# Performance work log

Hardware: AMD Instinct MI355X
Metric: run time of the kernel (lower is better)

The kernel has to match this reference:

```python
import jax, jax.numpy as jnp
import numpy as np

B, LAT, FCON, NCOND = 1024, 64, 256, 1
HID, E, GATE_H = 512, 8, 64
FREC, NFUT = 256, 2
IN_SZ = LAT + FCON * NCOND          # 320
INTER = LAT + HID                   # 576
OUT_SZ = NFUT * FREC                # 512


def setup_inputs() -> dict:
    key = jax.random.key(0)
    ks = jax.random.split(key, 16)

    def kaiming(k, shape):
        # kaiming_uniform over fan_in = shape[-2] (matches torch init on [E, in, out])
        fan_in = shape[-2]
        bound = np.sqrt(6.0 / fan_in)
        return jax.random.uniform(k, shape, jnp.float32, -bound, bound)

    def lin(kw, kb, din, dout):
        bound = 1.0 / np.sqrt(din)
        w = jax.random.uniform(kw, (din, dout), jnp.float32, -bound, bound)
        b = jax.random.uniform(kb, (dout,), jnp.float32, -bound, bound)
        return w, b

    gw1, gb1 = lin(ks[0], ks[1], IN_SZ, GATE_H)
    gw2, gb2 = lin(ks[2], ks[3], GATE_H, GATE_H)
    gw3, gb3 = lin(ks[4], ks[5], GATE_H, E)

    return {
        "z": jax.random.normal(ks[6], (B, LAT), jnp.float32),
        "c": jax.random.normal(ks[7], (B, FCON * NCOND), jnp.float32),
        "w0": kaiming(ks[8], (E, IN_SZ, HID)),
        "b0": jnp.full((E, HID), 0.01, jnp.float32),
        "w1": kaiming(ks[9], (E, INTER, HID)),
        "b1": jnp.full((E, HID), 0.01, jnp.float32),
        "w2": kaiming(ks[10], (E, INTER, OUT_SZ)),
        "b2": jnp.full((E, OUT_SZ), 0.01, jnp.float32),
        "gw1": gw1, "gb1": gb1,
        "gw2": gw2, "gb2": gb2,
        "gw3": gw3, "gb3": gb3,
    }


def _moe_layer(coeff, z, layer_out, w, b, act):
    # math identical to: mixed_w = coeff @ flat(w); baddbmm(mixed_b, inp, mixed_w)
    # expressed as a fused contraction (no [B, in, out] materialization)
    inp = jnp.concatenate((z, layer_out), axis=1)          # [B, in]
    out = jnp.einsum('bi,eio,be->bo', inp, w, coeff)       # [B, out]
    out = out + coeff @ b                                  # mixed bias
    return act(out) if act is not None else out


def reference(z, c, w0, b0, w1, b1, w2, b2, gw1, gb1, gw2, gb2, gw3, gb3):
    x = jnp.concatenate((z, c), axis=1)                    # [B, IN_SZ]
    h = jax.nn.elu(x @ gw1 + gb1)
    h = jax.nn.elu(h @ gw2 + gb2)
    coeff = jax.nn.softmax(h @ gw3 + gb3, axis=1)          # [B, E]

    out = _moe_layer(coeff, z, c, w0, b0, jax.nn.elu)      # [B, HID]
    out = _moe_layer(coeff, z, out, w1, b1, jax.nn.elu)    # [B, HID]
    out = _moe_layer(coeff, z, out, w2, b2, None)          # [B, OUT_SZ]
    return out
```

## Files before the change

### kernel.cpp

```cpp
#include <hip/hip_runtime.h>
#include <hip/hip_bf16.h>
#include <stdint.h>
#include <math.h>

#define B_    1024
#define LAT   64
#define FCON  256
#define IN_SZ 320
#define HID   512
#define E_    8
#define GH    64
#define INTER 576
#define OUT_SZ 512
#define NTOT  4096
#define KI0   10
#define KI12  18

typedef __attribute__((ext_vector_type(8))) __bf16 bf16x8;
typedef __attribute__((ext_vector_type(4))) float  f32x4;

__device__ __forceinline__ float elu_f(float x) { return x > 0.f ? x : expf(x) - 1.f; }
__device__ __forceinline__ __bf16 to_bf16(float f) {
    __hip_bfloat16 h = __float2bfloat16(f);
    return *reinterpret_cast<__bf16*>(&h);
}


#define PREP_ZC   160
#define PREP_W0   (PREP_ZC + KI0 * 64)
#define PREP_W1   (PREP_W0 + KI12 * 64)
#define PREP_W2   (PREP_W1 + KI12 * 64)
#define PREP_ALL  (PREP_W2 + 256)

__device__ __forceinline__ void do_zcpack(
    int bx, const float* __restrict__ z, const float* __restrict__ c,
    bf16x8* __restrict__ Ap0, bf16x8* __restrict__ Ap1, bf16x8* __restrict__ Ap2)
{
    const int wid  = bx * 4 + (threadIdx.x >> 6);
    const int lane = threadIdx.x & 63, q = lane >> 4, r = lane & 15;
    bf16x8 v;
    if (wid < 128) {
        const int mi = wid >> 1, ki = wid & 1;
        const float* src = z + (size_t)(mi * 16 + r) * LAT + ki * 32 + q * 8;
        const f32x4 lo = *(const f32x4*)src, hi = *(const f32x4*)(src + 4);
#pragma unroll
        for (int j = 0; j < 4; j++) { v[j] = to_bf16(lo[j]); v[j + 4] = to_bf16(hi[j]); }
        Ap0[((size_t)mi * KI0  + ki) * 64 + lane] = v;
        Ap1[((size_t)mi * KI12 + ki) * 64 + lane] = v;
        Ap2[((size_t)mi * KI12 + ki) * 64 + lane] = v;
    } else {
        const int cid = wid - 128;
        const int mi = cid >> 3, ki = 2 + (cid & 7);
        const float* src = c + (size_t)(mi * 16 + r) * FCON + (ki - 2) * 32 + q * 8;
        const f32x4 lo = *(const f32x4*)src, hi = *(const f32x4*)(src + 4);
#pragma unroll
        for (int j = 0; j < 4; j++) { v[j] = to_bf16(lo[j]); v[j + 4] = to_bf16(hi[j]); }
        Ap0[((size_t)mi * KI0 + ki) * 64 + lane] = v;
    }
}

__device__ __forceinline__ void do_wpack(
    int f, const float* __restrict__ w, bf16x8* __restrict__ Wp, int KI)
{
    const int ki = f % KI;
    const int ni = (f / KI) * 4 + (threadIdx.x >> 6);
    const int lane = threadIdx.x & 63, q = lane >> 4, r = lane & 15;
    const int n = ni * 16 + r, e = n >> 9, o = n & 511;
    const int K = KI * 32;
    const float* src = w + (size_t)e * K * 512 + (size_t)(ki * 32 + q * 8) * 512 + o;
    bf16x8 v;
#pragma unroll
    for (int j = 0; j < 8; j++) v[j] = to_bf16(src[(size_t)j * 512]);
    Wp[((size_t)ni * KI + ki) * 64 + lane] = v;
}

__global__ __launch_bounds__(256) void prep_kernel(
    const float* __restrict__ z, const float* __restrict__ c,
    const float* __restrict__ w0, const float* __restrict__ w1,
    const float* __restrict__ w2,
    const float* __restrict__ gw1, const float* __restrict__ gb1,
    const float* __restrict__ gw2, const float* __restrict__ gb2,
    const float* __restrict__ gw3, const float* __restrict__ gb3,
    bf16x8* __restrict__ Ap0, bf16x8* __restrict__ Ap1, bf16x8* __restrict__ Ap2,
    bf16x8* __restrict__ Wp0, bf16x8* __restrict__ Wp1, bf16x8* __restrict__ Wp2,
    float* __restrict__ coeff)
{
    const int bx = blockIdx.x;
    if (bx < PREP_ZC) {
        do_zcpack(bx, z, c, Ap0, Ap1, Ap2);
    } else if (bx < PREP_W0) {
        do_wpack(bx - PREP_ZC, w0, Wp0, KI0);
    } else if (bx < PREP_W1) {
        do_wpack(bx - PREP_W0, w1, Wp1, KI12);
    } else if (bx < PREP_W2) {
        do_wpack(bx - PREP_W1, w2, Wp2, KI12);
    } else {
        __shared__ float h[4][GH];
        __shared__ float lg[4][E_];
        const int lane = threadIdx.x & 63, wave = threadIdx.x >> 6;
        const int row = (bx - PREP_W2) * 4 + wave;
        const float* zr = z + (size_t)row * LAT;
        const float* cr = c + (size_t)row * FCON;

        float a1 = gb1[lane];
        for (int i = 0; i < LAT; i++)  a1 = fmaf(zr[i], gw1[i * GH + lane], a1);
        for (int i = 0; i < FCON; i++) a1 = fmaf(cr[i], gw1[(LAT + i) * GH + lane], a1);
        h[wave][lane] = elu_f(a1);
        __syncthreads();

        float a2 = gb2[lane];
        for (int i = 0; i < GH; i++) a2 = fmaf(h[wave][i], gw2[i * GH + lane], a2);
        a2 = elu_f(a2);
        __syncthreads();
        h[wave][lane] = a2;
        __syncthreads();

        if (lane < E_) {
            float a3 = gb3[lane];
            for (int i = 0; i < GH; i++) a3 = fmaf(h[wave][i], gw3[i * E_ + lane], a3);
            lg[wave][lane] = a3;
        }
        __syncthreads();
        if (lane < E_) {
            float mx = lg[wave][0];
            for (int i = 1; i < E_; i++) mx = fmaxf(mx, lg[wave][i]);
            float s = 0.f;
            for (int i = 0; i < E_; i++) s += expf(lg[wave][i] - mx);
            coeff[(size_t)row * E_ + lane] = expf(lg[wave][lane] - mx) / s;
        }
    }
}

template<int KI, int FINAL>
__global__ __launch_bounds__(256) void layer_kernel(
    const bf16x8* __restrict__ Ap, const bf16x8* __restrict__ Wp,
    const float* __restrict__ coeff, const float* __restrict__ bias,
    __bf16* __restrict__ ApN, float* __restrict__ fout)
{
    const int lane = threadIdx.x & 63, w = threadIdx.x >> 6;
    const int q = lane >> 4, r = lane & 15;
    const int o0 = blockIdx.x * 16;
    const int nt = blockIdx.x;
    const int mi0 = blockIdx.y * 8 + w * 2;

    const bf16x8* aB0 = Ap + (size_t)(mi0 + 0) * KI * 64 + lane;
    const bf16x8* aB1 = Ap + (size_t)(mi0 + 1) * KI * 64 + lane;
    const bf16x8* bBase = Wp + (size_t)nt * KI * 64 + lane;

    f32x4 acc[2][E_];
#pragma unroll
    for (int u = 0; u < 2; u++)
#pragma unroll
        for (int e = 0; e < E_; e++) acc[u][e] = (f32x4){0.f, 0.f, 0.f, 0.f};

#pragma unroll
    for (int ki = 0; ki < KI; ++ki) {
        const bf16x8 af0 = aB0[(size_t)ki * 64];
        const bf16x8 af1 = aB1[(size_t)ki * 64];
        bf16x8 bf[E_];
#pragma unroll
        for (int e = 0; e < E_; e++)
            bf[e] = bBase[((size_t)e * 32 * KI + ki) * 64];
#pragma unroll
        for (int e = 0; e < E_; e++) {
            acc[0][e] = __builtin_amdgcn_mfma_f32_16x16x32_bf16(af0, bf[e], acc[0][e], 0, 0, 0);
            acc[1][e] = __builtin_amdgcn_mfma_f32_16x16x32_bf16(af1, bf[e], acc[1][e], 0, 0, 0);
        }
    }

    float be[E_];
#pragma unroll
    for (int e = 0; e < E_; e++) be[e] = bias[(size_t)e * 512 + o0 + r];

#pragma unroll
    for (int u = 0; u < 2; u++) {
        const int mi = mi0 + u;
#pragma unroll
        for (int v = 0; v < 4; v++) {
            const int row = mi * 16 + q * 4 + v;
            const float* cr = coeff + (size_t)row * E_;
            const f32x4 clo = *(const f32x4*)cr, chi = *(const f32x4*)(cr + 4);
            float s = 0.f;
#pragma unroll
            for (int e = 0; e < 4; e++) s += clo[e] * (acc[u][e][v] + be[e]);
#pragma unroll
            for (int e = 0; e < 4; e++) s += chi[e] * (acc[u][4 + e][v] + be[4 + e]);
            if (FINAL) {
                fout[(size_t)row * OUT_SZ + o0 + r] = s;
            } else {
                const float h = elu_f(s);
                const int k  = LAT + o0 + r;
                const int ki2 = k >> 5, kq2 = (k & 31) >> 3, jb2 = k & 7;
                ApN[(((size_t)mi * KI12 + ki2) * 64 + kq2 * 16 + (q * 4 + v)) * 8 + jb2] =
                    to_bf16(h);
            }
        }
    }
}

static inline size_t align256(size_t x) { return (x + 255) & ~(size_t)255; }

extern "C" void kernel_launch(void* const* d_in, const int* in_sizes, int n_in,
                              void* d_out, int out_size, void* d_ws, size_t ws_size,
                              hipStream_t stream)
{
    const float* z   = (const float*)d_in[0];
    const float* c   = (const float*)d_in[1];
    const float* w0  = (const float*)d_in[2];
    const float* b0  = (const float*)d_in[3];
    const float* w1  = (const float*)d_in[4];
    const float* b1  = (const float*)d_in[5];
    const float* w2  = (const float*)d_in[6];
    const float* b2  = (const float*)d_in[7];
    const float* gw1 = (const float*)d_in[8];
    const float* gb1 = (const float*)d_in[9];
    const float* gw2 = (const float*)d_in[10];
    const float* gb2 = (const float*)d_in[11];
    const float* gw3 = (const float*)d_in[12];
    const float* gb3 = (const float*)d_in[13];
    float* out = (float*)d_out;

    uint8_t* p = (uint8_t*)d_ws;
    bf16x8* Wp0 = (bf16x8*)p; p += align256((size_t)NTOT * IN_SZ * 2);
    bf16x8* Wp1 = (bf16x8*)p; p += align256((size_t)NTOT * INTER * 2);
    bf16x8* Wp2 = (bf16x8*)p; p += align256((size_t)NTOT * INTER * 2);
    bf16x8* Ap0 = (bf16x8*)p; p += align256((size_t)B_ * IN_SZ * 2);
    bf16x8* Ap1 = (bf16x8*)p; p += align256((size_t)B_ * INTER * 2);
    bf16x8* Ap2 = (bf16x8*)p; p += align256((size_t)B_ * INTER * 2);
    float* coeff = (float*)p; p += align256((size_t)B_ * E_ * 4);

    prep_kernel<<<PREP_ALL, 256, 0, stream>>>(
        z, c, w0, w1, w2, gw1, gb1, gw2, gb2, gw3, gb3,
        Ap0, Ap1, Ap2, Wp0, Wp1, Wp2, coeff);

    layer_kernel<KI0, 0><<<dim3(32, 8), 256, 0, stream>>>(
        Ap0, Wp0, coeff, b0, (__bf16*)Ap1, nullptr);
    layer_kernel<KI12, 0><<<dim3(32, 8), 256, 0, stream>>>(
        Ap1, Wp1, coeff, b1, (__bf16*)Ap2, nullptr);
    layer_kernel<KI12, 1><<<dim3(32, 8), 256, 0, stream>>>(
        Ap2, Wp2, coeff, b2, nullptr, out);
}
```

Measured before the change: 156.8 us.

## Coalesce weight packing via LDS transpose, batch gate rows, split-K layers

The weight-packing pass now loads 32x256 fp32 tiles with coalesced vector loads into padded LDS and transposes from there, replacing strided scalar global reads. The gating MLP processes 16 rows per block from staged LDS input, uses four accumulators per weight load, and does the softmax with shuffles. Each layer kernel doubles its threads and splits K across wave pairs, reducing the partial sums through LDS, to raise occupancy and latency hiding. The cost is an extra barrier and LDS traffic per layer and a larger LDS footprint in the prep kernel.

```diff
diff --git a/kernel.cpp b/kernel.cpp
--- a/kernel.cpp
+++ b/kernel.cpp
@@ -26,11 +26,15 @@
 }
 
 
-#define PREP_ZC   160
-#define PREP_W0   (PREP_ZC + KI0 * 64)
-#define PREP_W1   (PREP_W0 + KI12 * 64)
-#define PREP_W2   (PREP_W1 + KI12 * 64)
-#define PREP_ALL  (PREP_W2 + 256)
+#define PREP_GATE 64
+#define PREP_ZC   (PREP_GATE + 160)
+#define PREP_W0   (PREP_ZC + 8 * KI0 * 2)
+#define PREP_W1   (PREP_W0 + 8 * KI12 * 2)
+#define PREP_W2   (PREP_W1 + 8 * KI12 * 2)
+#define PREP_ALL  PREP_W2
+
+#define WPAD 261
+#define SMEM_F (32 * WPAD)
 
 __device__ __forceinline__ void do_zcpack(
     int bx, const float* __restrict__ z, const float* __restrict__ c,
@@ -59,19 +63,120 @@
     }
 }
 
-__device__ __forceinline__ void do_wpack(
-    int f, const float* __restrict__ w, bf16x8* __restrict__ Wp, int KI)
-{
-    const int ki = f % KI;
-    const int ni = (f / KI) * 4 + (threadIdx.x >> 6);
-    const int lane = threadIdx.x & 63, q = lane >> 4, r = lane & 15;
-    const int n = ni * 16 + r, e = n >> 9, o = n & 511;
+__device__ __forceinline__ void do_wpack2(
+    int f, const float* __restrict__ w, bf16x8* __restrict__ Wp, int KI,
+    float* __restrict__ lds)
+{
+    const int e = f / (2 * KI), rem = f % (2 * KI);
+    const int ki = rem >> 1, ot2 = rem & 1;
     const int K = KI * 32;
-    const float* src = w + (size_t)e * K * 512 + (size_t)(ki * 32 + q * 8) * 512 + o;
-    bf16x8 v;
-#pragma unroll
-    for (int j = 0; j < 8; j++) v[j] = to_bf16(src[(size_t)j * 512]);
-    Wp[((size_t)ni * KI + ki) * 64 + lane] = v;
+    const float* base = w + ((size_t)e * K + ki * 32) * 512 + ot2 * 256;
+
+#pragma unroll
+    for (int p = 0; p < 8; ++p) {
+        const int idx = p * 256 + threadIdx.x;
+        const int kl = idx >> 6, c4 = idx & 63;
+        const f32x4 v = *(const f32x4*)(base + (size_t)kl * 512 + c4 * 4);
+        float* d = lds + kl * WPAD + c4 * 4;
+        d[0] = v[0]; d[1] = v[1]; d[2] = v[2]; d[3] = v[3];
+    }
+    __syncthreads();
+
+    const int wv = threadIdx.x >> 6, lane = threadIdx.x & 63;
+    const int q = lane >> 4, r = lane & 15;
+#pragma unroll
+    for (int ff = 0; ff < 4; ++ff) {
+        const int fo = wv * 4 + ff;
+        const int ol = fo * 16 + r;
+        bf16x8 v;
+#pragma unroll
+        for (int j = 0; j < 8; ++j) v[j] = to_bf16(lds[(q * 8 + j) * WPAD + ol]);
+        const int ni = e * 32 + ot2 * 16 + fo;
+        Wp[((size_t)ni * KI + ki) * 64 + lane] = v;
+    }
+}
+
+__device__ __forceinline__ void do_gate(
+    int bx, const float* __restrict__ z, const float* __restrict__ c,
+    const float* __restrict__ gw1, const float* __restrict__ gb1,
+    const float* __restrict__ gw2, const float* __restrict__ gb2,
+    const float* __restrict__ gw3, const float* __restrict__ gb3,
+    float* __restrict__ coeff, float* __restrict__ smem)
+{
+    float* xs = smem;
+    float* h  = smem + 16 * 320;
+    const int r0 = bx * 16;
+    const int wave = threadIdx.x >> 6, lane = threadIdx.x & 63;
+
+#pragma unroll
+    for (int p = 0; p < 5; ++p) {
+        const int idx = p * 256 + threadIdx.x;
+        const int row = idx / 80, c4 = idx % 80;
+        const float* src = (c4 < 16)
+            ? (z + (size_t)(r0 + row) * LAT  + c4 * 4)
+            : (c + (size_t)(r0 + row) * FCON + (c4 - 16) * 4);
+        *(f32x4*)(xs + row * 320 + c4 * 4) = *(const f32x4*)src;
+    }
+    __syncthreads();
+
+    float a0, a1, a2, a3;
+    {
+        const float b = gb1[lane];
+        a0 = b; a1 = b; a2 = b; a3 = b;
+        const float* x0 = xs + (wave * 4 + 0) * 320;
+        const float* x1 = xs + (wave * 4 + 1) * 320;
+        const float* x2 = xs + (wave * 4 + 2) * 320;
+        const float* x3 = xs + (wave * 4 + 3) * 320;
+#pragma unroll 8
+        for (int i = 0; i < IN_SZ; ++i) {
+            const float wv = gw1[i * GH + lane];
+            a0 = fmaf(x0[i], wv, a0);
+            a1 = fmaf(x1[i], wv, a1);
+            a2 = fmaf(x2[i], wv, a2);
+            a3 = fmaf(x3[i], wv, a3);
+        }
+        h[(wave * 4 + 0) * GH + lane] = elu_f(a0);
+        h[(wave * 4 + 1) * GH + lane] = elu_f(a1);
+        h[(wave * 4 + 2) * GH + lane] = elu_f(a2);
+        h[(wave * 4 + 3) * GH + lane] = elu_f(a3);
+    }
+    {
+        const float b = gb2[lane];
+        a0 = b; a1 = b; a2 = b; a3 = b;
+        const float* h0 = h + (wave * 4 + 0) * GH;
+        const float* h1 = h + (wave * 4 + 1) * GH;
+        const float* h2 = h + (wave * 4 + 2) * GH;
+        const float* h3 = h + (wave * 4 + 3) * GH;
+#pragma unroll 8
+        for (int i = 0; i < GH; ++i) {
+            const float wv = gw2[i * GH + lane];
+            a0 = fmaf(h0[i], wv, a0);
+            a1 = fmaf(h1[i], wv, a1);
+            a2 = fmaf(h2[i], wv, a2);
+            a3 = fmaf(h3[i], wv, a3);
+        }
+        h[(wave * 4 + 0) * GH + lane] = elu_f(a0);
+        h[(wave * 4 + 1) * GH + lane] = elu_f(a1);
+        h[(wave * 4 + 2) * GH + lane] = elu_f(a2);
+        h[(wave * 4 + 3) * GH + lane] = elu_f(a3);
+    }
+    if (lane < 32) {
+        const int rloc = lane >> 3, e = lane & 7;
+        const float* hr = h + (wave * 4 + rloc) * GH;
+        float lg = gb3[e];
+#pragma unroll 8
+        for (int i = 0; i < GH; ++i) lg = fmaf(hr[i], gw3[i * E_ + e], lg);
+        float mx = lg;
+        mx = fmaxf(mx, __shfl_xor(mx, 1, 8));
+        mx = fmaxf(mx, __shfl_xor(mx, 2, 8));
+        mx = fmaxf(mx, __shfl_xor(mx, 4, 8));
+        const float ex = expf(lg - mx);
+        float sm = ex;
+        sm += __shfl_xor(sm, 1, 8);
+        sm += __shfl_xor(sm, 2, 8);
+        sm += __shfl_xor(sm, 4, 8);
+        coeff[(size_t)(r0 + wave * 4 + rloc) * E_ + e] = ex / sm;
+    }
 }
 
 __global__ __launch_bounds__(256) void prep_kernel(
@@ -85,67 +190,39 @@
     bf16x8* __restrict__ Wp0, bf16x8* __restrict__ Wp1, bf16x8* __restrict__ Wp2,
     float* __restrict__ coeff)
 {
+    __shared__ float smem[SMEM_F];
     const int bx = blockIdx.x;
-    if (bx < PREP_ZC) {
-        do_zcpack(bx, z, c, Ap0, Ap1, Ap2);
+    if (bx < PREP_GATE) {
+        do_gate(bx, z, c, gw1, gb1, gw2, gb2, gw3, gb3, coeff, smem);
+    } else if (bx < PREP_ZC) {
+        do_zcpack(bx - PREP_GATE, z, c, Ap0, Ap1, Ap2);
     } else if (bx < PREP_W0) {
-        do_wpack(bx - PREP_ZC, w0, Wp0, KI0);
+        do_wpack2(bx - PREP_ZC, w0, Wp0, KI0, smem);
     } else if (bx < PREP_W1) {
-        do_wpack(bx - PREP_W0, w1, Wp1, KI12);
-    } else if (bx < PREP_W2) {
-        do_wpack(bx - PREP_W1, w2, Wp2, KI12);
+        do_wpack2(bx - PREP_W0, w1, Wp1, KI12, smem);
     } else {
-        __shared__ float h[4][GH];
-        __shared__ float lg[4][E_];
-        const int lane = threadIdx.x & 63, wave = threadIdx.x >> 6;
-        const int row = (bx - PREP_W2) * 4 + wave;
-        const float* zr = z + (size_t)row * LAT;
-        const float* cr = c + (size_t)row * FCON;
-
-        float a1 = gb1[lane];
-        for (int i = 0; i < LAT; i++)  a1 = fmaf(zr[i], gw1[i * GH + lane], a1);
-        for (int i = 0; i < FCON; i++) a1 = fmaf(cr[i], gw1[(LAT + i) * GH + lane], a1);
-        h[wave][lane] = elu_f(a1);
-        __syncthreads();
-
-        float a2 = gb2[lane];
-        for (int i = 0; i < GH; i++) a2 = fmaf(h[wave][i], gw2[i * GH + lane], a2);
-        a2 = elu_f(a2);
-        __syncthreads();
-        h[wave][lane] = a2;
-        __syncthreads();
-
-        if (lane < E_) {
-            float a3 = gb3[lane];
-            for (int i = 0; i < GH; i++) a3 = fmaf(h[wave][i], gw3[i * E_ + lane], a3);
-            lg[wave][lane] = a3;
-        }
-        __syncthreads();
-        if (lane < E_) {
-            float mx = lg[wave][0];
-            for (int i = 1; i < E_; i++) mx = fmaxf(mx, lg[wave][i]);
-            float s = 0.f;
-            for (int i = 0; i < E_; i++) s += expf(lg[wave][i] - mx);
-            coeff[(size_t)row * E_ + lane] = expf(lg[wave][lane] - mx) / s;
-        }
+        do_wpack2(bx - PREP_W1, w2, Wp2, KI12, smem);
     }
 }
 
 template<int KI, int FINAL>
-__global__ __launch_bounds__(256) void layer_kernel(
+__global__ __launch_bounds__(512) void layer_kernel(
     const bf16x8* __restrict__ Ap, const bf16x8* __restrict__ Wp,
     const float* __restrict__ coeff, const float* __restrict__ bias,
     __bf16* __restrict__ ApN, float* __restrict__ fout)
 {
+    constexpr int KIH = KI / 2;
+    __shared__ float sbuf[4][8][64];
     const int lane = threadIdx.x & 63, w = threadIdx.x >> 6;
+    const int kh = w & 1, pp = w >> 1;
     const int q = lane >> 4, r = lane & 15;
     const int o0 = blockIdx.x * 16;
     const int nt = blockIdx.x;
-    const int mi0 = blockIdx.y * 8 + w * 2;
-
-    const bf16x8* aB0 = Ap + (size_t)(mi0 + 0) * KI * 64 + lane;
-    const bf16x8* aB1 = Ap + (size_t)(mi0 + 1) * KI * 64 + lane;
-    const bf16x8* bBase = Wp + (size_t)nt * KI * 64 + lane;
+    const int mi0 = blockIdx.y * 8 + pp * 2;
+
+    const bf16x8* aB0 = Ap + ((size_t)(mi0 + 0) * KI + kh * KIH) * 64 + lane;
+    const bf16x8* aB1 = Ap + ((size_t)(mi0 + 1) * KI + kh * KIH) * 64 + lane;
+    const bf16x8* bB  = Wp + ((size_t)nt * KI + kh * KIH) * 64 + lane;
 
     f32x4 acc[2][E_];
 #pragma unroll
@@ -154,13 +231,13 @@
         for (int e = 0; e < E_; e++) acc[u][e] = (f32x4){0.f, 0.f, 0.f, 0.f};
 
 #pragma unroll
-    for (int ki = 0; ki < KI; ++ki) {
+    for (int ki = 0; ki < KIH; ++ki) {
         const bf16x8 af0 = aB0[(size_t)ki * 64];
         const bf16x8 af1 = aB1[(size_t)ki * 64];
         bf16x8 bf[E_];
 #pragma unroll
         for (int e = 0; e < E_; e++)
-            bf[e] = bBase[((size_t)e * 32 * KI + ki) * 64];
+            bf[e] = bB[((size_t)e * 32 * KI + ki) * 64];
 #pragma unroll
         for (int e = 0; e < E_; e++) {
             acc[0][e] = __builtin_amdgcn_mfma_f32_16x16x32_bf16(af0, bf[e], acc[0][e], 0, 0, 0);
@@ -170,29 +247,50 @@
 
     float be[E_];
 #pragma unroll
-    for (int e = 0; e < E_; e++) be[e] = bias[(size_t)e * 512 + o0 + r];
-
+    for (int e = 0; e < E_; e++)
+        be[e] = kh ? 0.f : bias[(size_t)e * 512 + o0 + r];
+
+    float s[2][4];
 #pragma unroll
     for (int u = 0; u < 2; u++) {
-        const int mi = mi0 + u;
 #pragma unroll
         for (int v = 0; v < 4; v++) {
-            const int row = mi * 16 + q * 4 + v;
+            const int row = (mi0 + u) * 16 + q * 4 + v;
             const float* cr = coeff + (size_t)row * E_;
             const f32x4 clo = *(const f32x4*)cr, chi = *(const f32x4*)(cr + 4);
-            float s = 0.f;
-#pragma unroll
-            for (int e = 0; e < 4; e++) s += clo[e] * (acc[u][e][v] + be[e]);
-#pragma unroll
-            for (int e = 0; e < 4; e++) s += chi[e] * (acc[u][4 + e][v] + be[4 + e]);
-            if (FINAL) {
-                fout[(size_t)row * OUT_SZ + o0 + r] = s;
-            } else {
-                const float h = elu_f(s);
-                const int k  = LAT + o0 + r;
-                const int ki2 = k >> 5, kq2 = (k & 31) >> 3, jb2 = k & 7;
-                ApN[(((size_t)mi * KI12 + ki2) * 64 + kq2 * 16 + (q * 4 + v)) * 8 + jb2] =
-                    to_bf16(h);
+            float sv = 0.f;
+#pragma unroll
+            for (int e = 0; e < 4; e++) sv += clo[e] * (acc[u][e][v] + be[e]);
+#pragma unroll
+            for (int e = 0; e < 4; e++) sv += chi[e] * (acc[u][4 + e][v] + be[4 + e]);
+            s[u][v] = sv;
+        }
+    }
+
+    if (kh) {
+#pragma unroll
+        for (int u = 0; u < 2; u++)
+#pragma unroll
+            for (int v = 0; v < 4; v++) sbuf[pp][u * 4 + v][lane] = s[u][v];
+    }
+    __syncthreads();
+    if (!kh) {
+#pragma unroll
+        for (int u = 0; u < 2; u++) {
+            const int mi = mi0 + u;
+#pragma unroll
+            for (int v = 0; v < 4; v++) {
+                const int row = mi * 16 + q * 4 + v;
+                const float t = s[u][v] + sbuf[pp][u * 4 + v][lane];
+                if (FINAL) {
+                    fout[(size_t)row * OUT_SZ + o0 + r] = t;
+                } else {
+                    const float hh = elu_f(t);
+                    const int k  = LAT + o0 + r;
+                    const int ki2 = k >> 5, kq2 = (k & 31) >> 3, jb2 = k & 7;
+                    ApN[(((size_t)mi * KI12 + ki2) * 64 + kq2 * 16 + (q * 4 + v)) * 8 + jb2] =
+                        to_bf16(hh);
+                }
             }
         }
     }
@@ -233,10 +331,10 @@
         z, c, w0, w1, w2, gw1, gb1, gw2, gb2, gw3, gb3,
         Ap0, Ap1, Ap2, Wp0, Wp1, Wp2, coeff);
 
-    layer_kernel<KI0, 0><<<dim3(32, 8), 256, 0, stream>>>(
+    layer_kernel<KI0, 0><<<dim3(32, 8), 512, 0, stream>>>(
         Ap0, Wp0, coeff, b0, (__bf16*)Ap1, nullptr);
-    layer_kernel<KI12, 0><<<dim3(32, 8), 256, 0, stream>>>(
+    layer_kernel<KI12, 0><<<dim3(32, 8), 512, 0, stream>>>(
         Ap1, Wp1, coeff, b1, (__bf16*)Ap2, nullptr);
-    layer_kernel<KI12, 1><<<dim3(32, 8), 256, 0, stream>>>(
+    layer_kernel<KI12, 1><<<dim3(32, 8), 512, 0, stream>>>(
         Ap2, Wp2, coeff, b2, nullptr, out);
 }
```

Measured after the change: 161.0 us. 2.7% more time.
